# Optimization experiments

Measured on AMD Instinct MI355X. Metric: run time of the kernel, lower is better.

Reference implementation:

```python
import jax, jax.numpy as jnp
import numpy as np

DIM = 1024
HEADS = 16
B, N = 4, 2048


def setup_inputs() -> dict:
    key = jax.random.key(0)
    ks = jax.random.split(key, 6)
    scale = DIM ** -0.5
    return {
        "x": jax.random.normal(ks[0], (B, N, DIM), dtype=jnp.float32),
        "mask": jax.random.randint(ks[1], (B, N, N), 0, 2) > 0,
        "Wqkv": jax.random.normal(ks[2], (DIM, 3 * DIM), dtype=jnp.float32) * scale,
        "bqkv": jax.random.normal(ks[3], (3 * DIM,), dtype=jnp.float32) * 0.02,
        "Wproj": jax.random.normal(ks[4], (DIM, DIM), dtype=jnp.float32) * scale,
        "bproj": jax.random.normal(ks[5], (DIM,), dtype=jnp.float32) * 0.02,
    }


def reference(x, mask, Wqkv, bqkv, Wproj, bproj):
    Bs, Ns, C = x.shape
    H = HEADS
    D = C // H
    scale = D ** -0.5
    qkv = x @ Wqkv + bqkv                       # [B, N, 3C]
    qkv = qkv.reshape(Bs, Ns, 3, H, D)          # split (three h d)
    q, k, v = jnp.moveaxis(qkv, 2, 0)           # each [B, N, H, D]
    q = q.transpose(0, 2, 1, 3)                 # [B, H, N, D]
    k = k.transpose(0, 2, 1, 3)
    v = v.transpose(0, 2, 1, 3)
    attn = jnp.einsum("bhnd,bhmd->bhnm", q, k) * scale  # [B, H, N, N]
    attn = jnp.where(mask[:, None, :, :], -jnp.inf, attn)
    attn = jax.nn.softmax(attn, axis=-1)
    out = jnp.einsum("bhnm,bhmd->bhnd", attn, v)        # [B, H, N, D]
    out = out.transpose(0, 2, 1, 3).reshape(Bs, Ns, C)  # [B, N, C]
    return out @ Wproj + bproj
```

## Files before the change

### kernel.cpp

```cpp
#include <hip/hip_runtime.h>
#include <cstdint>
#include <cstddef>

constexpr int kC = 1024;
constexpr int kH = 16;
constexpr int kB = 4;
constexpr int kN = 2048;
constexpr int kD = 64;

#define KQ_SCALE 0.18033688011112042f

typedef unsigned short u16;
typedef unsigned int   u32;
typedef unsigned long long u64;
typedef __bf16 v8bf  __attribute__((ext_vector_type(8)));
typedef __bf16 v4bf  __attribute__((ext_vector_type(4)));
typedef float  v4f   __attribute__((ext_vector_type(4)));
typedef u16    u16x8 __attribute__((ext_vector_type(8)));
typedef u16    u16x4 __attribute__((ext_vector_type(4)));
typedef u32    u32x4 __attribute__((ext_vector_type(4)));

__device__ inline u16 f2bf(float f) {
    union { float f; unsigned u; } v; v.f = f;
    unsigned r = v.u + 0x7FFFu + ((v.u >> 16) & 1u);
    return (u16)(r >> 16);
}

__device__ inline float fast_exp2(float x) {
#if __has_builtin(__builtin_amdgcn_exp2f)
    return __builtin_amdgcn_exp2f(x);
#else
    return __expf(x * 0.6931471805599453f);
#endif
}

__device__ inline void gl2lds16(const u16* g, u16* l) {
    __builtin_amdgcn_global_load_lds(
        (const __attribute__((address_space(1))) void*)g,
        (__attribute__((address_space(3))) void*)l, 16, 0, 0);
}

__global__ __launch_bounds__(256) void cast_bf16_kernel(
    const float* __restrict__ in, u16* __restrict__ outp)
{
    const int i = blockIdx.x * 256 + threadIdx.x;
    const float4 f = ((const float4*)in)[i];
    u16x4 o;
    o.x = f2bf(f.x); o.y = f2bf(f.y); o.z = f2bf(f.z); o.w = f2bf(f.w);
    ((u16x4*)outp)[i] = o;
}

__global__ __launch_bounds__(256) void tpose_cast_kernel(
    const float* __restrict__ W, u16* __restrict__ Wt, int R, int Cc)
{
    __shared__ u16 tile[64][65];
    const int c0 = blockIdx.x * 64;
    const int r0 = blockIdx.y * 64;
    const int t  = threadIdx.x;
#pragma unroll
    for (int it = 0; it < 16; ++it) {
        const int r = it * 4 + (t >> 6);
        const int c = t & 63;
        tile[c][r] = f2bf(W[(size_t)(r0 + r) * Cc + c0 + c]);
    }
    __syncthreads();
#pragma unroll
    for (int it = 0; it < 16; ++it) {
        const int rr = it * 4 + (t >> 6);
        const int cc = t & 63;
        Wt[(size_t)(c0 + rr) * R + r0 + cc] = tile[rr][cc];
    }
}

__global__ __launch_bounds__(256) void maskpack_kernel(
    const int* __restrict__ mask, u32* __restrict__ bits)
{
    const int lane = threadIdx.x & 63;
    const int wv   = threadIdx.x >> 6;
    const int nseg = kB * kN * 32;
    for (int seg = blockIdx.x * 4 + wv; seg < nseg; seg += gridDim.x * 4) {
        const size_t row = (size_t)(seg >> 5);
        const int s = seg & 31;
        const int m = mask[row * kN + s * 64 + lane];
        const u64 bal = __ballot(m != 0);
        if (lane == 0) ((u64*)bits)[row * 32 + s] = bal;
    }
}

template <int MODE>
__global__ __launch_bounds__(256, 3) void gemm_mfma_kernel(
    const u16* __restrict__ A, const u16* __restrict__ Bt,
    const float* __restrict__ bias, float* __restrict__ Cout,
    u16* __restrict__ qOut, u16* __restrict__ kOut, u16* __restrict__ vOut,
    int M, int N, int K)
{
    __shared__ u16 As0[128 * 32], Bs0[128 * 32];
    __shared__ u16 As1[128 * 32], Bs1[128 * 32];
    __shared__ u16 As2[128 * 32], Bs2[128 * 32];
    const int t    = threadIdx.x;
    const int w    = t >> 6;
    const int lane = t & 63;
    const int quad = lane >> 4;
    const int l16  = lane & 15;

    const int nby = M >> 7;
    const int q8  = (int)gridDim.x >> 3;
    const int bid = (int)blockIdx.x;
    const int swz = (bid & 7) * q8 + (bid >> 3);
    const int m0  = (swz % nby) * 128;
    const int n0  = (swz / nby) * 128;

    const int sr  = lane >> 2;
    const int scs = ((lane & 3) ^ ((sr >> 1) & 3)) * 8;
    const u16* Ag0 = A  + (size_t)(m0 + 32 * w      + sr) * K + scs;
    const u16* Ag1 = A  + (size_t)(m0 + 32 * w + 16 + sr) * K + scs;
    const u16* Bg0 = Bt + (size_t)(n0 + 32 * w      + sr) * K + scs;
    const u16* Bg1 = Bt + (size_t)(n0 + 32 * w + 16 + sr) * K + scs;

    v4f acc[4][4];
#pragma unroll
    for (int r = 0; r < 4; ++r)
#pragma unroll
        for (int c = 0; c < 4; ++c) acc[r][c] = (v4f){0.f, 0.f, 0.f, 0.f};

    const int mrow = (w >> 1) * 64;
    const int ncol = (w & 1) * 64;
    const int pch  = (quad ^ ((l16 >> 1) & 3)) * 8;

    auto stage = [&](u16* Asb, u16* Bsb, int k0) {
        gl2lds16(Ag0 + k0, Asb + (32 * w) * 32);
        gl2lds16(Ag1 + k0, Asb + (32 * w + 16) * 32);
        gl2lds16(Bg0 + k0, Bsb + (32 * w) * 32);
        gl2lds16(Bg1 + k0, Bsb + (32 * w + 16) * 32);
    };
    auto compute = [&](const u16* Asb, const u16* Bsb) {
        v8bf af[4], bfr[4];
#pragma unroll
        for (int r = 0; r < 4; ++r)
            af[r] = *(const v8bf*)(Asb + (mrow + r * 16 + l16) * 32 + pch);
#pragma unroll
        for (int c = 0; c < 4; ++c)
            bfr[c] = *(const v8bf*)(Bsb + (ncol + c * 16 + l16) * 32 + pch);
        __builtin_amdgcn_s_setprio(1);
#pragma unroll
        for (int r = 0; r < 4; ++r)
#pragma unroll
            for (int c = 0; c < 4; ++c)
                acc[r][c] = __builtin_amdgcn_mfma_f32_16x16x32_bf16(
                    af[r], bfr[c], acc[r][c], 0, 0, 0);
        __builtin_amdgcn_s_setprio(0);
    };

    stage(As0, Bs0, 0);
    stage(As1, Bs1, 32);
    u16 *pa0 = As0, *pb0 = Bs0, *pa1 = As1, *pb1 = Bs1, *pa2 = As2, *pb2 = Bs2;

    for (int k0 = 0; k0 < K; k0 += 32) {
        if (k0 + 32 < K) {
            asm volatile("s_waitcnt vmcnt(4)" ::: "memory");
        } else {
            asm volatile("s_waitcnt vmcnt(0)" ::: "memory");
        }
        __builtin_amdgcn_s_barrier();
        __builtin_amdgcn_sched_barrier(0);
        if (k0 + 64 < K) stage(pa2, pb2, k0 + 64);
        compute(pa0, pb0);
        u16* ta = pa0; pa0 = pa1; pa1 = pa2; pa2 = ta;
        u16* tb = pb0; pb0 = pb1; pb1 = pb2; pb2 = tb;
    }

#pragma unroll
    for (int r = 0; r < 4; ++r) {
#pragma unroll
        for (int c = 0; c < 4; ++c) {
            const int col = n0 + ncol + c * 16 + l16;
            const float bv = bias[col];
#pragma unroll
            for (int reg = 0; reg < 4; ++reg) {
                const int row = m0 + mrow + r * 16 + quad * 4 + reg;
                float val = acc[r][c][reg] + bv;
                if (MODE == 0) {
                    Cout[(size_t)row * N + col] = val;
                } else {
                    const int which = col >> 10;
                    const int rem   = col & 1023;
                    const int h     = rem >> 6;
                    const int d     = rem & 63;
                    const int b     = row >> 11;
                    const int n     = row & 2047;
                    if (which == 0) val *= KQ_SCALE;
                    u16* dst = (which == 0) ? qOut : (which == 1) ? kOut : vOut;
                    dst[(((size_t)(b * kH + h)) * kN + n) * kD + d] = f2bf(val);
                }
            }
        }
    }
}

__global__ __launch_bounds__(256, 2) void attn_mfma_kernel(
    const u16* __restrict__ q, const u16* __restrict__ k,
    const u16* __restrict__ v, const u32* __restrict__ mbits,
    u16* __restrict__ out)
{
    __shared__ u16 Ks[2][128 * 64];
    __shared__ u16 Vt[2][64 * 128];

    const int t    = threadIdx.x;
    const int w    = t >> 6;
    const int lane = t & 63;
    const int quad = lane >> 4;
    const int l16  = lane & 15;

    const int bh    = blockIdx.x >> 4;
    const int tile0 = (blockIdx.x & 15) * 128;
    const int b     = bh >> 4;
    const int h     = bh & 15;

    const u16* qb = q + (size_t)bh * kN * kD;
    const u16* kb = k + (size_t)bh * kN * kD;
    const u16* vb = v + (size_t)bh * kN * kD;

    const int qrow0 = tile0 + w * 32 + l16;
    const int qrow1 = qrow0 + 16;
    v8bf qf[2][2];
    qf[0][0] = *(const v8bf*)(qb + (size_t)qrow0 * kD + quad * 8);
    qf[0][1] = *(const v8bf*)(qb + (size_t)qrow0 * kD + 32 + quad * 8);
    qf[1][0] = *(const v8bf*)(qb + (size_t)qrow1 * kD + quad * 8);
    qf[1][1] = *(const v8bf*)(qb + (size_t)qrow1 * kD + 32 + quad * 8);

    const int skr  = t >> 1;
    const int skh  = t & 1;
    const int vg   = t >> 4;
    const int vdq  = t & 15;
    const int vrow0 = (vg >> 2) * 32 + (vg & 3) * 4;

    const u16* kp = kb + (size_t)skr * kD + skh * 32;
    const u16* vp = vb + (size_t)vrow0 * kD + vdq * 4;
    const uint4* mp0 = (const uint4*)(mbits + ((size_t)b * kN + qrow0) * 64);
    const uint4* mp1 = (const uint4*)(mbits + ((size_t)b * kN + qrow1) * 64);

    u16x8 kpre[4];
    u16x4 vpre[8];
    uint4 mpre0, mpre1;
    auto issue_prefetch = [&]() {
#pragma unroll
        for (int i = 0; i < 4; ++i)
            kpre[i] = *(const u16x8*)(kp + i * 8);
#pragma unroll
        for (int i = 0; i < 8; ++i)
            vpre[i] = *(const u16x4*)(vp + (i < 4 ? i * 64 : 1024 + (i - 4) * 64));
        mpre0 = *mp0; mpre1 = *mp1;
        kp += 128 * kD; vp += 128 * kD; ++mp0; ++mp1;
    };

    v8bf onesf;
#pragma unroll
    for (int j = 0; j < 8; ++j) onesf[j] = (__bf16)1.0f;

    v4f oacc[2][4];
    v4f rsacc[2];
#pragma unroll
    for (int qs = 0; qs < 2; ++qs) {
        rsacc[qs] = (v4f){0.f, 0.f, 0.f, 0.f};
#pragma unroll
        for (int i = 0; i < 4; ++i) oacc[qs][i] = (v4f){0.f, 0.f, 0.f, 0.f};
    }

    issue_prefetch();

    for (int kt = 0; kt < kN / 128; ++kt) {
        u16* KsB = Ks[kt & 1];
        u16* VtB = Vt[kt & 1];

        {
            const int cb = skh * 4;
            u16* drow = &KsB[skr * 64];
#pragma unroll
            for (int i = 0; i < 4; ++i)
                *(u16x8*)(&drow[((cb + i) ^ (skr & 7)) * 8]) = kpre[i];
        }
        {
#pragma unroll
            for (int dd = 0; dd < 4; ++dd) {
                const int d = vdq * 4 + dd;
                u16x8 col;
#pragma unroll
                for (int j = 0; j < 8; ++j) col[j] = vpre[j][dd];
                *(u16x8*)(&VtB[d * 128 + ((vg ^ (d & 15)) * 8)]) = col;
            }
        }
        const uint4 mc0 = mpre0, mc1 = mpre1;
        if (kt + 1 < kN / 128) issue_prefetch();

        __syncthreads();

        const u32 mwa[2][4] = {{mc0.x, mc0.y, mc0.z, mc0.w},
                               {mc1.x, mc1.y, mc1.z, mc1.w}};
        v8bf pa[2][4];

#pragma unroll
        for (int nb = 0; nb < 8; ++nb) {
            const int krow = nb * 16 + l16;
            const v8bf kf0 = *(const v8bf*)(&KsB[krow * 64 + ((quad       ^ (krow & 7)) * 8)]);
            const v8bf kf1 = *(const v8bf*)(&KsB[krow * 64 + (((quad + 4) ^ (krow & 7)) * 8)]);
#pragma unroll
            for (int qs = 0; qs < 2; ++qs) {
                v4f s = (v4f){0.f, 0.f, 0.f, 0.f};
                s = __builtin_amdgcn_mfma_f32_16x16x32_bf16(kf0, qf[qs][0], s, 0, 0, 0);
                s = __builtin_amdgcn_mfma_f32_16x16x32_bf16(kf1, qf[qs][1], s, 0, 0, 0);

                const u32 m4 = (mwa[qs][nb >> 1] >> ((nb & 1) * 16 + quad * 4)) & 0xFu;
                float e0 = fast_exp2(s[0]);
                float e1 = fast_exp2(s[1]);
                float e2 = fast_exp2(s[2]);
                float e3 = fast_exp2(s[3]);
                e0 = (m4 & 1u) ? 0.f : e0;
                e1 = (m4 & 2u) ? 0.f : e1;
                e2 = (m4 & 4u) ? 0.f : e2;
                e3 = (m4 & 8u) ? 0.f : e3;

                pa[qs][nb >> 1][(nb & 1) * 4 + 0] = (__bf16)e0;
                pa[qs][nb >> 1][(nb & 1) * 4 + 1] = (__bf16)e1;
                pa[qs][nb >> 1][(nb & 1) * 4 + 2] = (__bf16)e2;
                pa[qs][nb >> 1][(nb & 1) * 4 + 3] = (__bf16)e3;
            }
        }

        __builtin_amdgcn_s_setprio(1);
#pragma unroll
        for (int qs = 0; qs < 2; ++qs)
#pragma unroll
            for (int ks = 0; ks < 4; ++ks)
                rsacc[qs] = __builtin_amdgcn_mfma_f32_16x16x32_bf16(
                    pa[qs][ks], onesf, rsacc[qs], 0, 0, 0);
#pragma unroll
        for (int ks = 0; ks < 4; ++ks)
#pragma unroll
            for (int db = 0; db < 4; ++db) {
                const int d = db * 16 + l16;
                const v8bf vf = *(const v8bf*)(&VtB[d * 128 + (((ks * 4 + quad) ^ (d & 15)) * 8)]);
#pragma unroll
                for (int qs = 0; qs < 2; ++qs)
                    oacc[qs][db] = __builtin_amdgcn_mfma_f32_16x16x32_bf16(
                        pa[qs][ks], vf, oacc[qs][db], 0, 0, 0);
            }
        __builtin_amdgcn_s_setprio(0);
    }

#pragma unroll
    for (int qs = 0; qs < 2; ++qs) {
        float inv[4];
#pragma unroll
        for (int reg = 0; reg < 4; ++reg) inv[reg] = 1.f / rsacc[qs][reg];
#pragma unroll
        for (int db = 0; db < 4; ++db)
#pragma unroll
            for (int reg = 0; reg < 4; ++reg) {
                const int row = tile0 + w * 32 + qs * 16 + quad * 4 + reg;
                const int col = h * 64 + db * 16 + l16;
                out[((size_t)(b * kN + row)) * kC + col] = f2bf(oacc[qs][db][reg] * inv[reg]);
            }
    }
}

extern "C" void kernel_launch(void* const* d_in, const int* in_sizes, int n_in,
                              void* d_out, int out_size, void* d_ws, size_t ws_size,
                              hipStream_t stream)
{
    const float* x     = (const float*)d_in[0];
    const int*   mask  = (const int*)d_in[1];
    const float* Wqkv  = (const float*)d_in[2];
    const float* bqkv  = (const float*)d_in[3];
    const float* Wproj = (const float*)d_in[4];
    const float* bproj = (const float*)d_in[5];
    float* out = (float*)d_out;

    const size_t nx = (size_t)kB * kN * kC;
    const size_t qkv_elems = (size_t)kB * kH * kN * kD;
    u16* xb     = (u16*)d_ws;
    u16* qbuf   = xb + nx;
    u16* kbuf   = qbuf + qkv_elems;
    u16* vbuf   = kbuf + qkv_elems;
    u16* aob    = vbuf + qkv_elems;
    u16* Wqkvt  = aob + nx;
    u16* Wprojt = Wqkvt + (size_t)3 * kC * kC;
    u32* mbits  = (u32*)(Wprojt + (size_t)kC * kC);

    maskpack_kernel<<<dim3(2048), dim3(256), 0, stream>>>(mask, mbits);
    cast_bf16_kernel<<<dim3(nx / 1024), dim3(256), 0, stream>>>(x, xb);
    tpose_cast_kernel<<<dim3(3 * kC / 64, kC / 64), dim3(256), 0, stream>>>(
        Wqkv, Wqkvt, kC, 3 * kC);
    tpose_cast_kernel<<<dim3(kC / 64, kC / 64), dim3(256), 0, stream>>>(
        Wproj, Wprojt, kC, kC);

    gemm_mfma_kernel<1><<<dim3((3 * kC / 128) * (kB * kN / 128)), dim3(256), 0, stream>>>(
        xb, Wqkvt, bqkv, nullptr, qbuf, kbuf, vbuf, kB * kN, 3 * kC, kC);

    attn_mfma_kernel<<<dim3(kB * kH * (kN / 128)), dim3(256), 0, stream>>>(
        qbuf, kbuf, vbuf, mbits, aob);

    gemm_mfma_kernel<0><<<dim3((kC / 128) * (kB * kN / 128)), dim3(256), 0, stream>>>(
        aob, Wprojt, bproj, out, nullptr, nullptr, nullptr, kB * kN, kC, kC);
}
```

Before: 361.1 us.

## Double attention query tile to 256 rows per block for K/V reuse

Each attention block now handles 256 query rows instead of 128: every wave processes four 16-row query subtiles instead of two. Each K/V tile staged in LDS is therefore reused across twice as many queries, which halves global K/V traffic and LDS staging work per query. In exchange register pressure roughly doubles (accumulators, P fragments, mask words), which risks spills or lower occupancy under launch_bounds(256,2), and the grid drops to 512 blocks.

```diff
diff --git a/kernel.cpp b/kernel.cpp
--- a/kernel.cpp
+++ b/kernel.cpp
@@ -14,11 +14,9 @@
 typedef unsigned int   u32;
 typedef unsigned long long u64;
 typedef __bf16 v8bf  __attribute__((ext_vector_type(8)));
-typedef __bf16 v4bf  __attribute__((ext_vector_type(4)));
 typedef float  v4f   __attribute__((ext_vector_type(4)));
 typedef u16    u16x8 __attribute__((ext_vector_type(8)));
 typedef u16    u16x4 __attribute__((ext_vector_type(4)));
-typedef u32    u32x4 __attribute__((ext_vector_type(4)));
 
 __device__ inline u16 f2bf(float f) {
     union { float f; unsigned u; } v; v.f = f;
@@ -211,8 +209,8 @@
     const int quad = lane >> 4;
     const int l16  = lane & 15;
 
-    const int bh    = blockIdx.x >> 4;
-    const int tile0 = (blockIdx.x & 15) * 128;
+    const int bh    = blockIdx.x >> 3;
+    const int tile0 = (blockIdx.x & 7) * 256;
     const int b     = bh >> 4;
     const int h     = bh & 15;
 
@@ -220,13 +218,13 @@
     const u16* kb = k + (size_t)bh * kN * kD;
     const u16* vb = v + (size_t)bh * kN * kD;
 
-    const int qrow0 = tile0 + w * 32 + l16;
-    const int qrow1 = qrow0 + 16;
-    v8bf qf[2][2];
-    qf[0][0] = *(const v8bf*)(qb + (size_t)qrow0 * kD + quad * 8);
-    qf[0][1] = *(const v8bf*)(qb + (size_t)qrow0 * kD + 32 + quad * 8);
-    qf[1][0] = *(const v8bf*)(qb + (size_t)qrow1 * kD + quad * 8);
-    qf[1][1] = *(const v8bf*)(qb + (size_t)qrow1 * kD + 32 + quad * 8);
+    v8bf qf[4][2];
+#pragma unroll
+    for (int qs = 0; qs < 4; ++qs) {
+        const int qrow = tile0 + w * 64 + qs * 16 + l16;
+        qf[qs][0] = *(const v8bf*)(qb + (size_t)qrow * kD + quad * 8);
+        qf[qs][1] = *(const v8bf*)(qb + (size_t)qrow * kD + 32 + quad * 8);
+    }
 
     const int skr  = t >> 1;
     const int skh  = t & 1;
@@ -236,12 +234,15 @@
 
     const u16* kp = kb + (size_t)skr * kD + skh * 32;
     const u16* vp = vb + (size_t)vrow0 * kD + vdq * 4;
-    const uint4* mp0 = (const uint4*)(mbits + ((size_t)b * kN + qrow0) * 64);
-    const uint4* mp1 = (const uint4*)(mbits + ((size_t)b * kN + qrow1) * 64);
+    const uint4* mp[4];
+#pragma unroll
+    for (int qs = 0; qs < 4; ++qs)
+        mp[qs] = (const uint4*)(mbits +
+            ((size_t)b * kN + tile0 + w * 64 + qs * 16 + l16) * 64);
 
     u16x8 kpre[4];
     u16x4 vpre[8];
-    uint4 mpre0, mpre1;
+    uint4 mpre[4];
     auto issue_prefetch = [&]() {
 #pragma unroll
         for (int i = 0; i < 4; ++i)
@@ -249,18 +250,19 @@
 #pragma unroll
         for (int i = 0; i < 8; ++i)
             vpre[i] = *(const u16x4*)(vp + (i < 4 ? i * 64 : 1024 + (i - 4) * 64));
-        mpre0 = *mp0; mpre1 = *mp1;
-        kp += 128 * kD; vp += 128 * kD; ++mp0; ++mp1;
+#pragma unroll
+        for (int qs = 0; qs < 4; ++qs) { mpre[qs] = *mp[qs]; ++mp[qs]; }
+        kp += 128 * kD; vp += 128 * kD;
     };
 
     v8bf onesf;
 #pragma unroll
     for (int j = 0; j < 8; ++j) onesf[j] = (__bf16)1.0f;
 
-    v4f oacc[2][4];
-    v4f rsacc[2];
-#pragma unroll
-    for (int qs = 0; qs < 2; ++qs) {
+    v4f oacc[4][4];
+    v4f rsacc[4];
+#pragma unroll
+    for (int qs = 0; qs < 4; ++qs) {
         rsacc[qs] = (v4f){0.f, 0.f, 0.f, 0.f};
 #pragma unroll
         for (int i = 0; i < 4; ++i) oacc[qs][i] = (v4f){0.f, 0.f, 0.f, 0.f};
@@ -289,14 +291,20 @@
                 *(u16x8*)(&VtB[d * 128 + ((vg ^ (d & 15)) * 8)]) = col;
             }
         }
-        const uint4 mc0 = mpre0, mc1 = mpre1;
+        uint4 mc[4];
+#pragma unroll
+        for (int qs = 0; qs < 4; ++qs) mc[qs] = mpre[qs];
         if (kt + 1 < kN / 128) issue_prefetch();
 
         __syncthreads();
 
-        const u32 mwa[2][4] = {{mc0.x, mc0.y, mc0.z, mc0.w},
-                               {mc1.x, mc1.y, mc1.z, mc1.w}};
-        v8bf pa[2][4];
+        u32 mwa[4][4];
+#pragma unroll
+        for (int qs = 0; qs < 4; ++qs) {
+            mwa[qs][0] = mc[qs].x; mwa[qs][1] = mc[qs].y;
+            mwa[qs][2] = mc[qs].z; mwa[qs][3] = mc[qs].w;
+        }
+        v8bf pa[4][4];
 
 #pragma unroll
         for (int nb = 0; nb < 8; ++nb) {
@@ -304,7 +312,7 @@
             const v8bf kf0 = *(const v8bf*)(&KsB[krow * 64 + ((quad       ^ (krow & 7)) * 8)]);
             const v8bf kf1 = *(const v8bf*)(&KsB[krow * 64 + (((quad + 4) ^ (krow & 7)) * 8)]);
 #pragma unroll
-            for (int qs = 0; qs < 2; ++qs) {
+            for (int qs = 0; qs < 4; ++qs) {
                 v4f s = (v4f){0.f, 0.f, 0.f, 0.f};
                 s = __builtin_amdgcn_mfma_f32_16x16x32_bf16(kf0, qf[qs][0], s, 0, 0, 0);
                 s = __builtin_amdgcn_mfma_f32_16x16x32_bf16(kf1, qf[qs][1], s, 0, 0, 0);
@@ -328,7 +336,7 @@
 
         __builtin_amdgcn_s_setprio(1);
 #pragma unroll
-        for (int qs = 0; qs < 2; ++qs)
+        for (int qs = 0; qs < 4; ++qs)
 #pragma unroll
             for (int ks = 0; ks < 4; ++ks)
                 rsacc[qs] = __builtin_amdgcn_mfma_f32_16x16x32_bf16(
@@ -340,7 +348,7 @@
                 const int d = db * 16 + l16;
                 const v8bf vf = *(const v8bf*)(&VtB[d * 128 + (((ks * 4 + quad) ^ (d & 15)) * 8)]);
 #pragma unroll
-                for (int qs = 0; qs < 2; ++qs)
+                for (int qs = 0; qs < 4; ++qs)
                     oacc[qs][db] = __builtin_amdgcn_mfma_f32_16x16x32_bf16(
                         pa[qs][ks], vf, oacc[qs][db], 0, 0, 0);
             }
@@ -348,7 +356,7 @@
     }
 
 #pragma unroll
-    for (int qs = 0; qs < 2; ++qs) {
+    for (int qs = 0; qs < 4; ++qs) {
         float inv[4];
 #pragma unroll
         for (int reg = 0; reg < 4; ++reg) inv[reg] = 1.f / rsacc[qs][reg];
@@ -356,7 +364,7 @@
         for (int db = 0; db < 4; ++db)
 #pragma unroll
             for (int reg = 0; reg < 4; ++reg) {
-                const int row = tile0 + w * 32 + qs * 16 + quad * 4 + reg;
+                const int row = tile0 + w * 64 + qs * 16 + quad * 4 + reg;
                 const int col = h * 64 + db * 16 + l16;
                 out[((size_t)(b * kN + row)) * kC + col] = f2bf(oacc[qs][db][reg] * inv[reg]);
             }
@@ -396,7 +404,7 @@
     gemm_mfma_kernel<1><<<dim3((3 * kC / 128) * (kB * kN / 128)), dim3(256), 0, stream>>>(
         xb, Wqkvt, bqkv, nullptr, qbuf, kbuf, vbuf, kB * kN, 3 * kC, kC);
 
-    attn_mfma_kernel<<<dim3(kB * kH * (kN / 128)), dim3(256), 0, stream>>>(
+    attn_mfma_kernel<<<dim3(kB * kH * (kN / 256)), dim3(256), 0, stream>>>(
         qbuf, kbuf, vbuf, mbits, aob);
 
     gemm_mfma_kernel<0><<<dim3((kC / 128) * (kB * kN / 128)), dim3(256), 0, stream>>>(
```

New measurement: 399.2 us. +10.6%, slower.
